# Performance work log

Measured on AMD Instinct MI355X. Metric: run time of the kernel, lower is better.

Reference implementation:

```python
import jax, jax.numpy as jnp
import numpy as np

N, M, H, DIN, DOUT = 65536, 512, 1024, 512, 512
EPS = 1e-8


def setup_inputs() -> dict:
    key = jax.random.key(0)
    ks = jax.random.split(key, 24)
    s = 0.02  # weight init scale
    f32 = jnp.float32
    inp = {
        "x": jax.random.normal(ks[0], (DIN,), f32),
        "h0": jax.random.normal(ks[1], (H,), f32),
        "c0": jax.random.normal(ks[2], (H,), f32),
        "memory": jax.random.normal(ks[3], (N, M), f32),
        "read_vec": jax.random.normal(ks[4], (M,), f32),
        # LSTMCell params (torch layout: gates ordered i, f, g, o)
        "W_ih": jax.random.normal(ks[5], (4 * H, DIN + M), f32) * s,
        "b_ih": jax.random.normal(ks[6], (4 * H,), f32) * s,
        "W_hh": jax.random.normal(ks[7], (4 * H, H), f32) * s,
        "b_hh": jax.random.normal(ks[8], (4 * H,), f32) * s,
        # output head
        "W_fc": jax.random.normal(ks[9], (DOUT, H), f32) * s,
        "b_fc": jax.random.normal(ks[10], (DOUT,), f32) * s,
        # addressing / write heads
        "W_key": jax.random.normal(ks[11], (M, H), f32) * s,
        "b_key": jax.random.normal(ks[12], (M,), f32) * s,
        "W_beta": jax.random.normal(ks[13], (1, H), f32) * s,
        "b_beta": jax.random.normal(ks[14], (1,), f32) * s,
        "W_erase": jax.random.normal(ks[15], (M, H), f32) * s,
        "b_erase": jax.random.normal(ks[16], (M,), f32) * s,
        "W_add": jax.random.normal(ks[17], (M, H), f32) * s,
        "b_add": jax.random.normal(ks[18], (M,), f32) * s,
    }
    return inp


def reference(x, h0, c0, memory, read_vec,
              W_ih, b_ih, W_hh, b_hh, W_fc, b_fc,
              W_key, b_key, W_beta, b_beta,
              W_erase, b_erase, W_add, b_add):
    # controller input: cat([x, prev read vector])  -> [DIN + M]
    xi = jnp.concatenate([x, read_vec])
    # LSTMCell (torch gate order i, f, g, o)
    gates = W_ih @ xi + b_ih + W_hh @ h0 + b_hh  # [4H]
    i, f, g, o = jnp.split(gates, 4)
    i = jax.nn.sigmoid(i)
    f = jax.nn.sigmoid(f)
    g = jnp.tanh(g)
    o = jax.nn.sigmoid(o)
    c = f * c0 + i * g
    h = o * jnp.tanh(c)
    out = jax.nn.sigmoid(W_fc @ h + b_fc)  # sigmoid(controller_out)

    # content addressing on the PRE-write memory
    kvec = jnp.tanh(W_key @ h + b_key)                       # [M]
    beta = jax.nn.softplus(W_beta @ h + b_beta) + EPS        # [1]
    kn = kvec / (jnp.linalg.norm(kvec) + EPS)                # global-norm key (as in source)
    mem_norm = memory / (jnp.linalg.norm(memory, axis=1, keepdims=True) + EPS)  # [N,M]
    sim = mem_norm @ kn                                       # [N]
    w = jax.nn.softmax(beta * sim)                            # [N]

    # write (erase then add), then read from the UPDATED memory
    erase = jax.nn.sigmoid(W_erase @ h + b_erase)             # [M]
    add = jnp.tanh(W_add @ h + b_add)                         # [M]
    mem_new = memory * (1.0 - w[:, None] * erase[None, :]) + w[:, None] * add[None, :]
    read_new = w @ mem_new                                    # [M]
    return (out, h, c, mem_new, read_new)
```

## Files before the change

kernel.cpp:

```cpp
#include <hip/hip_runtime.h>
#include <math.h>

#define N_ROWS 65536
#define M_DIM  512
#define H_DIM  1024
#define EPS    1e-8f
#define NBLK_U 2048
#define NBLK_S 2048

typedef float f32x4 __attribute__((ext_vector_type(4)));

__device__ __forceinline__ float sigmoidf_(float v) { return 1.f / (1.f + expf(-v)); }

#define WS_KVEC  0
#define WS_ERASE 512
#define WS_ADD   1024
#define WS_SCAL  1536
#define WS_P     2048
#define WS_PSUM  67584
#define WS_PART  69632
#define WS_OUT1  1118208

__global__ void __launch_bounds__(256) k_gatecell(
        const float* __restrict__ x, const float* __restrict__ rv,
        const float* __restrict__ h0, const float* __restrict__ c0,
        const float* __restrict__ W_ih, const float* __restrict__ b_ih,
        const float* __restrict__ W_hh, const float* __restrict__ b_hh,
        float* __restrict__ h_out, float* __restrict__ c_out) {
    __shared__ float gval[4];
    int j = blockIdx.x;
    int wid = threadIdx.x >> 6;
    int lane = threadIdx.x & 63;
    int r = wid * H_DIM + j;
    const float4* Wi = (const float4*)(W_ih + (size_t)r * 1024);
    const float4* Wh = (const float4*)(W_hh + (size_t)r * 1024);
    const float4* xv = (const float4*)x;
    const float4* rvv = (const float4*)rv;
    const float4* hv = (const float4*)h0;
    float s = 0.f;
#pragma unroll
    for (int k = 0; k < 4; ++k) {
        int idx = k * 64 + lane;
        float4 wiv = Wi[idx];
        float4 in4 = (k < 2) ? xv[idx] : rvv[idx - 128];
        s += wiv.x * in4.x + wiv.y * in4.y + wiv.z * in4.z + wiv.w * in4.w;
        float4 whv = Wh[idx];
        float4 h4 = hv[idx];
        s += whv.x * h4.x + whv.y * h4.y + whv.z * h4.z + whv.w * h4.w;
    }
#pragma unroll
    for (int o = 32; o > 0; o >>= 1) s += __shfl_xor(s, o);
    if (lane == 0) gval[wid] = s + b_ih[r] + b_hh[r];
    __syncthreads();
    if (threadIdx.x == 0) {
        float ig = sigmoidf_(gval[0]);
        float fg = sigmoidf_(gval[1]);
        float gg = tanhf(gval[2]);
        float og = sigmoidf_(gval[3]);
        float c = fg * c0[j] + ig * gg;
        float h = og * tanhf(c);
        c_out[j] = c;
        h_out[j] = h;
    }
}

__global__ void __launch_bounds__(256) k_heads(
        const float* __restrict__ h,
        const float* __restrict__ W_fc, const float* __restrict__ b_fc,
        const float* __restrict__ W_key, const float* __restrict__ b_key,
        const float* __restrict__ W_beta, const float* __restrict__ b_beta,
        const float* __restrict__ W_erase, const float* __restrict__ b_erase,
        const float* __restrict__ W_add, const float* __restrict__ b_add,
        float* __restrict__ out, float* __restrict__ kvec,
        float* __restrict__ scal, float* __restrict__ erase,
        float* __restrict__ addv) {
    int wave = (blockIdx.x * blockDim.x + threadIdx.x) >> 6;
    int lane = threadIdx.x & 63;
    if (wave >= 2049) return;
    const float* Wrow;
    float bias;
    int kind, r;
    if (wave < 512)        { kind = 0; r = wave;        Wrow = W_fc    + (size_t)r * 1024; bias = b_fc[r]; }
    else if (wave < 1024)  { kind = 1; r = wave - 512;  Wrow = W_key   + (size_t)r * 1024; bias = b_key[r]; }
    else if (wave == 1024) { kind = 2; r = 0;           Wrow = W_beta;                     bias = b_beta[0]; }
    else if (wave < 1537)  { kind = 3; r = wave - 1025; Wrow = W_erase + (size_t)r * 1024; bias = b_erase[r]; }
    else                   { kind = 4; r = wave - 1537; Wrow = W_add   + (size_t)r * 1024; bias = b_add[r]; }
    const float4* Wv = (const float4*)Wrow;
    const float4* hv = (const float4*)h;
    float s = 0.f;
#pragma unroll
    for (int k = 0; k < 4; ++k) {
        int idx = k * 64 + lane;
        float4 w4 = Wv[idx];
        float4 h4 = hv[idx];
        s += w4.x * h4.x + w4.y * h4.y + w4.z * h4.z + w4.w * h4.w;
    }
#pragma unroll
    for (int o = 32; o > 0; o >>= 1) s += __shfl_xor(s, o);
    if (lane == 0) {
        float v = s + bias;
        if (kind == 0)      out[r]   = sigmoidf_(v);
        else if (kind == 1) kvec[r]  = tanhf(v);
        else if (kind == 2) scal[0]  = v;
        else if (kind == 3) erase[r] = sigmoidf_(v);
        else                addv[r]  = tanhf(v);
    }
}

__global__ void __launch_bounds__(256) k_simexp(
        const float* __restrict__ mem, const float* __restrict__ kvec,
        const float* __restrict__ scal,
        float* __restrict__ p, float* __restrict__ psum) {
    __shared__ float red[256];
    __shared__ float skn[512];
    __shared__ float wsum[4];
    int t = threadIdx.x;
    float v0 = kvec[t];
    float v1 = kvec[t + 256];
    red[t] = v0 * v0 + v1 * v1;
    __syncthreads();
#pragma unroll
    for (int s2 = 128; s2 > 0; s2 >>= 1) {
        if (t < s2) red[t] += red[t + s2];
        __syncthreads();
    }
    float invn = 1.f / (sqrtf(red[0]) + EPS);
    float braw = scal[0];
    float beta = ((braw > 20.f) ? braw : log1pf(expf(braw))) + EPS;
    skn[t] = v0 * invn;
    skn[t + 256] = v1 * invn;
    __syncthreads();
    int wid = t >> 6, lane = t & 63;
    float4 k0 = ((const float4*)skn)[lane];
    float4 k1 = ((const float4*)skn)[64 + lane];
    int gw = blockIdx.x * 4 + wid;
    size_t base = (size_t)gw * 8;
    float lsum = 0.f;
#pragma unroll 2
    for (int i = 0; i < 8; ++i) {
        size_t row = base + i;
        const float4* mv = (const float4*)(mem + row * M_DIM);
        float4 m0 = mv[lane];
        float4 m1 = mv[64 + lane];
        float dot = m0.x * k0.x + m0.y * k0.y + m0.z * k0.z + m0.w * k0.w
                  + m1.x * k1.x + m1.y * k1.y + m1.z * k1.z + m1.w * k1.w;
        float ss  = m0.x * m0.x + m0.y * m0.y + m0.z * m0.z + m0.w * m0.w
                  + m1.x * m1.x + m1.y * m1.y + m1.z * m1.z + m1.w * m1.w;
#pragma unroll
        for (int o = 32; o > 0; o >>= 1) {
            dot += __shfl_xor(dot, o);
            ss  += __shfl_xor(ss, o);
        }
        float pe = expf(beta * (dot / (sqrtf(ss) + EPS)));
        if (lane == 0) {
            p[row] = pe;
            lsum += pe;
        }
    }
    if (lane == 0) wsum[wid] = lsum;
    __syncthreads();
    if (t == 0) psum[blockIdx.x] = (wsum[0] + wsum[1]) + (wsum[2] + wsum[3]);
}

__global__ void __launch_bounds__(256) k_update(
        const float* __restrict__ mem, const float* __restrict__ p,
        const float* __restrict__ psum,
        const float* __restrict__ erase, const float* __restrict__ addv,
        float* __restrict__ mem_out, float* __restrict__ partial) {
    __shared__ float red[256];
    __shared__ float4 s_e[128];
    __shared__ float4 s_a[128];
    __shared__ float  s_w[32];
    __shared__ float4 s_red[128];
    int t = threadIdx.x;
    float s = 0.f;
#pragma unroll
    for (int i = 0; i < 8; ++i) s += psum[t + i * 256];
    red[t] = s;
    __syncthreads();
#pragma unroll
    for (int s2 = 128; s2 > 0; s2 >>= 1) {
        if (t < s2) red[t] += red[t + s2];
        __syncthreads();
    }
    float winv = 1.f / red[0];
    if (t < 128) {
        s_e[t] = ((const float4*)erase)[t];
        s_a[t] = ((const float4*)addv)[t];
    }
    int rowBase = blockIdx.x * 32;
    if (t < 32) s_w[t] = p[rowBase + t] * winv;
    __syncthreads();
    int sub = t >> 7;
    int c4  = t & 127;
    float4 e4 = s_e[c4];
    float4 a4 = s_a[c4];
    float4 acc = make_float4(0.f, 0.f, 0.f, 0.f);
#pragma unroll 4
    for (int it = 0; it < 16; ++it) {
        int row = rowBase + it * 2 + sub;
        float wr = s_w[it * 2 + sub];
        float4 m4 = ((const float4*)(mem + (size_t)row * M_DIM))[c4];
        f32x4 n4;
        n4.x = m4.x * (1.f - wr * e4.x) + wr * a4.x;
        n4.y = m4.y * (1.f - wr * e4.y) + wr * a4.y;
        n4.z = m4.z * (1.f - wr * e4.z) + wr * a4.z;
        n4.w = m4.w * (1.f - wr * e4.w) + wr * a4.w;
        __builtin_nontemporal_store(n4, (f32x4*)(mem_out + (size_t)row * M_DIM) + c4);
        acc.x += wr * n4.x;
        acc.y += wr * n4.y;
        acc.z += wr * n4.z;
        acc.w += wr * n4.w;
    }
    if (sub) s_red[c4] = acc;
    __syncthreads();
    if (!sub) {
        float4 o = s_red[c4];
        acc.x += o.x; acc.y += o.y; acc.z += o.z; acc.w += o.w;
        ((float4*)(partial + (size_t)blockIdx.x * M_DIM))[c4] = acc;
    }
}

__global__ void __launch_bounds__(256) k_red1(const float* __restrict__ partial,
                                              float* __restrict__ out1) {
    int g = blockIdx.x, t = threadIdx.x;
    float s0 = 0.f, s1 = 0.f;
    int b0 = g * 32;
#pragma unroll 4
    for (int b = b0; b < b0 + 32; ++b) {
        s0 += partial[(size_t)b * M_DIM + t];
        s1 += partial[(size_t)b * M_DIM + 256 + t];
    }
    out1[(size_t)g * M_DIM + t] = s0;
    out1[(size_t)g * M_DIM + 256 + t] = s1;
}

__global__ void __launch_bounds__(512) k_red2(const float* __restrict__ out1,
                                              float* __restrict__ read_new) {
    int t = threadIdx.x;
    float s = 0.f;
#pragma unroll 4
    for (int g = 0; g < 64; ++g) s += out1[(size_t)g * M_DIM + t];
    read_new[t] = s;
}

extern "C" void kernel_launch(void* const* d_in, const int* in_sizes, int n_in,
                              void* d_out, int out_size, void* d_ws, size_t ws_size,
                              hipStream_t stream) {
    const float* x        = (const float*)d_in[0];
    const float* h0       = (const float*)d_in[1];
    const float* c0       = (const float*)d_in[2];
    const float* memory   = (const float*)d_in[3];
    const float* read_vec = (const float*)d_in[4];
    const float* W_ih     = (const float*)d_in[5];
    const float* b_ih     = (const float*)d_in[6];
    const float* W_hh     = (const float*)d_in[7];
    const float* b_hh     = (const float*)d_in[8];
    const float* W_fc     = (const float*)d_in[9];
    const float* b_fc     = (const float*)d_in[10];
    const float* W_key    = (const float*)d_in[11];
    const float* b_key    = (const float*)d_in[12];
    const float* W_beta   = (const float*)d_in[13];
    const float* b_beta   = (const float*)d_in[14];
    const float* W_erase  = (const float*)d_in[15];
    const float* b_erase  = (const float*)d_in[16];
    const float* W_add    = (const float*)d_in[17];
    const float* b_add    = (const float*)d_in[18];

    float* out      = (float*)d_out;
    float* h_out    = out + 512;
    float* c_out    = h_out + 1024;
    float* mem_out  = c_out + 1024;
    float* read_out = mem_out + (size_t)N_ROWS * M_DIM;

    float* ws     = (float*)d_ws;
    float* kvec   = ws + WS_KVEC;
    float* erase  = ws + WS_ERASE;
    float* addv   = ws + WS_ADD;
    float* scal   = ws + WS_SCAL;
    float* p      = ws + WS_P;
    float* psum   = ws + WS_PSUM;
    float* part   = ws + WS_PART;
    float* out1   = ws + WS_OUT1;

    k_gatecell<<<1024, 256, 0, stream>>>(x, read_vec, h0, c0, W_ih, b_ih, W_hh, b_hh,
                                         h_out, c_out);
    k_heads<<<513, 256, 0, stream>>>(h_out, W_fc, b_fc, W_key, b_key, W_beta, b_beta,
                                     W_erase, b_erase, W_add, b_add,
                                     out, kvec, scal, erase, addv);
    k_simexp<<<NBLK_S, 256, 0, stream>>>(memory, kvec, scal, p, psum);
    k_update<<<NBLK_U, 256, 0, stream>>>(memory, p, psum, erase, addv, mem_out, part);
    k_red1<<<64, 256, 0, stream>>>(part, out1);
    k_red2<<<1, 512, 0, stream>>>(out1, read_out);
}
```

Measured before the change: 91.17 us.

## Compute read vector algebraically from pre-write memory during similarity pass

Expands read_new = w·mem_new into sum(p·m)/S - erase·sum(p²·m)/S² + add·sum(p²)/S², accumulating the two weighted row sums while memory is already loaded for the similarity pass. The update kernel becomes a pure streaming write with no reduction, and the final merge applies the normalisation. Similarity blocks now handle 16 rows each with more registers and shared memory, and rounding differs from the direct formula.

```diff
diff --git a/kernel.cpp b/kernel.cpp
--- a/kernel.cpp
+++ b/kernel.cpp
@@ -5,8 +5,8 @@
 #define M_DIM  512
 #define H_DIM  1024
 #define EPS    1e-8f
+#define NBLK_S 1024
 #define NBLK_U 2048
-#define NBLK_S 2048
 
 typedef float f32x4 __attribute__((ext_vector_type(4)));
 
@@ -18,8 +18,11 @@
 #define WS_SCAL  1536
 #define WS_P     2048
 #define WS_PSUM  67584
-#define WS_PART  69632
-#define WS_OUT1  1118208
+#define WS_P2SUM 68608
+#define WS_PART1 69632
+#define WS_PART2 593920
+#define WS_O1A   1118208
+#define WS_O1B   1150976
 
 __global__ void __launch_bounds__(256) k_gatecell(
         const float* __restrict__ x, const float* __restrict__ rv,
@@ -110,18 +113,22 @@
 __global__ void __launch_bounds__(256) k_simexp(
         const float* __restrict__ mem, const float* __restrict__ kvec,
         const float* __restrict__ scal,
-        float* __restrict__ p, float* __restrict__ psum) {
+        float* __restrict__ p, float* __restrict__ psum, float* __restrict__ p2sum,
+        float* __restrict__ part1, float* __restrict__ part2) {
     __shared__ float red[256];
     __shared__ float skn[512];
     __shared__ float wsum[4];
+    __shared__ float w2sum[4];
+    __shared__ float4 s1[4][128];
+    __shared__ float4 s2[4][128];
     int t = threadIdx.x;
     float v0 = kvec[t];
     float v1 = kvec[t + 256];
     red[t] = v0 * v0 + v1 * v1;
     __syncthreads();
 #pragma unroll
-    for (int s2 = 128; s2 > 0; s2 >>= 1) {
-        if (t < s2) red[t] += red[t + s2];
+    for (int s2_ = 128; s2_ > 0; s2_ >>= 1) {
+        if (t < s2_) red[t] += red[t + s2_];
         __syncthreads();
     }
     float invn = 1.f / (sqrtf(red[0]) + EPS);
@@ -133,11 +140,12 @@
     int wid = t >> 6, lane = t & 63;
     float4 k0 = ((const float4*)skn)[lane];
     float4 k1 = ((const float4*)skn)[64 + lane];
-    int gw = blockIdx.x * 4 + wid;
-    size_t base = (size_t)gw * 8;
-    float lsum = 0.f;
+    size_t base = ((size_t)blockIdx.x * 4 + wid) * 16;
+    float lsum = 0.f, l2sum = 0.f;
+    float4 a1lo = make_float4(0.f,0.f,0.f,0.f), a1hi = make_float4(0.f,0.f,0.f,0.f);
+    float4 a2lo = make_float4(0.f,0.f,0.f,0.f), a2hi = make_float4(0.f,0.f,0.f,0.f);
 #pragma unroll 2
-    for (int i = 0; i < 8; ++i) {
+    for (int i = 0; i < 16; ++i) {
         size_t row = base + i;
         const float4* mv = (const float4*)(mem + row * M_DIM);
         float4 m0 = mv[lane];
@@ -152,35 +160,61 @@
             ss  += __shfl_xor(ss, o);
         }
         float pe = expf(beta * (dot / (sqrtf(ss) + EPS)));
-        if (lane == 0) {
-            p[row] = pe;
-            lsum += pe;
-        }
-    }
-    if (lane == 0) wsum[wid] = lsum;
-    __syncthreads();
-    if (t == 0) psum[blockIdx.x] = (wsum[0] + wsum[1]) + (wsum[2] + wsum[3]);
+        if (lane == 0) p[row] = pe;
+        float pe2 = pe * pe;
+        lsum += pe;
+        l2sum += pe2;
+        a1lo.x += pe * m0.x;  a1lo.y += pe * m0.y;  a1lo.z += pe * m0.z;  a1lo.w += pe * m0.w;
+        a1hi.x += pe * m1.x;  a1hi.y += pe * m1.y;  a1hi.z += pe * m1.z;  a1hi.w += pe * m1.w;
+        a2lo.x += pe2 * m0.x; a2lo.y += pe2 * m0.y; a2lo.z += pe2 * m0.z; a2lo.w += pe2 * m0.w;
+        a2hi.x += pe2 * m1.x; a2hi.y += pe2 * m1.y; a2hi.z += pe2 * m1.z; a2hi.w += pe2 * m1.w;
+    }
+    s1[wid][lane] = a1lo;  s1[wid][64 + lane] = a1hi;
+    s2[wid][lane] = a2lo;  s2[wid][64 + lane] = a2hi;
+    if (lane == 0) { wsum[wid] = lsum; w2sum[wid] = l2sum; }
+    __syncthreads();
+    if (t < 128) {
+        float4 A = s1[0][t], B = s1[1][t], C = s1[2][t], D = s1[3][t];
+        float4 r4;
+        r4.x = (A.x + B.x) + (C.x + D.x);
+        r4.y = (A.y + B.y) + (C.y + D.y);
+        r4.z = (A.z + B.z) + (C.z + D.z);
+        r4.w = (A.w + B.w) + (C.w + D.w);
+        ((float4*)(part1 + (size_t)blockIdx.x * M_DIM))[t] = r4;
+    } else {
+        int u = t - 128;
+        float4 A = s2[0][u], B = s2[1][u], C = s2[2][u], D = s2[3][u];
+        float4 r4;
+        r4.x = (A.x + B.x) + (C.x + D.x);
+        r4.y = (A.y + B.y) + (C.y + D.y);
+        r4.z = (A.z + B.z) + (C.z + D.z);
+        r4.w = (A.w + B.w) + (C.w + D.w);
+        ((float4*)(part2 + (size_t)blockIdx.x * M_DIM))[u] = r4;
+    }
+    if (t == 0) {
+        psum[blockIdx.x]  = (wsum[0] + wsum[1]) + (wsum[2] + wsum[3]);
+        p2sum[blockIdx.x] = (w2sum[0] + w2sum[1]) + (w2sum[2] + w2sum[3]);
+    }
 }
 
 __global__ void __launch_bounds__(256) k_update(
         const float* __restrict__ mem, const float* __restrict__ p,
         const float* __restrict__ psum,
         const float* __restrict__ erase, const float* __restrict__ addv,
-        float* __restrict__ mem_out, float* __restrict__ partial) {
+        float* __restrict__ mem_out) {
     __shared__ float red[256];
     __shared__ float4 s_e[128];
     __shared__ float4 s_a[128];
     __shared__ float  s_w[32];
-    __shared__ float4 s_red[128];
     int t = threadIdx.x;
     float s = 0.f;
 #pragma unroll
-    for (int i = 0; i < 8; ++i) s += psum[t + i * 256];
+    for (int i = 0; i < 4; ++i) s += psum[t + i * 256];
     red[t] = s;
     __syncthreads();
 #pragma unroll
-    for (int s2 = 128; s2 > 0; s2 >>= 1) {
-        if (t < s2) red[t] += red[t + s2];
+    for (int s2_ = 128; s2_ > 0; s2_ >>= 1) {
+        if (t < s2_) red[t] += red[t + s2_];
         __syncthreads();
     }
     float winv = 1.f / red[0];
@@ -195,7 +229,6 @@
     int c4  = t & 127;
     float4 e4 = s_e[c4];
     float4 a4 = s_a[c4];
-    float4 acc = make_float4(0.f, 0.f, 0.f, 0.f);
 #pragma unroll 4
     for (int it = 0; it < 16; ++it) {
         int row = rowBase + it * 2 + sub;
@@ -207,41 +240,61 @@
         n4.z = m4.z * (1.f - wr * e4.z) + wr * a4.z;
         n4.w = m4.w * (1.f - wr * e4.w) + wr * a4.w;
         __builtin_nontemporal_store(n4, (f32x4*)(mem_out + (size_t)row * M_DIM) + c4);
-        acc.x += wr * n4.x;
-        acc.y += wr * n4.y;
-        acc.z += wr * n4.z;
-        acc.w += wr * n4.w;
-    }
-    if (sub) s_red[c4] = acc;
-    __syncthreads();
-    if (!sub) {
-        float4 o = s_red[c4];
-        acc.x += o.x; acc.y += o.y; acc.z += o.z; acc.w += o.w;
-        ((float4*)(partial + (size_t)blockIdx.x * M_DIM))[c4] = acc;
-    }
-}
-
-__global__ void __launch_bounds__(256) k_red1(const float* __restrict__ partial,
-                                              float* __restrict__ out1) {
+    }
+}
+
+__global__ void __launch_bounds__(256) k_merge1(
+        const float* __restrict__ part1, const float* __restrict__ part2,
+        float* __restrict__ o1a, float* __restrict__ o1b) {
     int g = blockIdx.x, t = threadIdx.x;
-    float s0 = 0.f, s1 = 0.f;
-    int b0 = g * 32;
+    float s0 = 0.f, s1 = 0.f, s2 = 0.f, s3 = 0.f;
+    int b0 = g * 16;
 #pragma unroll 4
-    for (int b = b0; b < b0 + 32; ++b) {
-        s0 += partial[(size_t)b * M_DIM + t];
-        s1 += partial[(size_t)b * M_DIM + 256 + t];
-    }
-    out1[(size_t)g * M_DIM + t] = s0;
-    out1[(size_t)g * M_DIM + 256 + t] = s1;
-}
-
-__global__ void __launch_bounds__(512) k_red2(const float* __restrict__ out1,
-                                              float* __restrict__ read_new) {
+    for (int b = b0; b < b0 + 16; ++b) {
+        s0 += part1[(size_t)b * M_DIM + t];
+        s1 += part1[(size_t)b * M_DIM + 256 + t];
+        s2 += part2[(size_t)b * M_DIM + t];
+        s3 += part2[(size_t)b * M_DIM + 256 + t];
+    }
+    o1a[(size_t)g * M_DIM + t] = s0;
+    o1a[(size_t)g * M_DIM + 256 + t] = s1;
+    o1b[(size_t)g * M_DIM + t] = s2;
+    o1b[(size_t)g * M_DIM + 256 + t] = s3;
+}
+
+__global__ void __launch_bounds__(512) k_merge2(
+        const float* __restrict__ o1a, const float* __restrict__ o1b,
+        const float* __restrict__ psum, const float* __restrict__ p2sum,
+        const float* __restrict__ erase, const float* __restrict__ addv,
+        float* __restrict__ read_new) {
+    __shared__ float red[512];
     int t = threadIdx.x;
-    float s = 0.f;
+    red[t] = psum[t] + psum[t + 512];
+    __syncthreads();
+#pragma unroll
+    for (int s2_ = 256; s2_ > 0; s2_ >>= 1) {
+        if (t < s2_) red[t] += red[t + s2_];
+        __syncthreads();
+    }
+    float sumP = red[0];
+    __syncthreads();
+    red[t] = p2sum[t] + p2sum[t + 512];
+    __syncthreads();
+#pragma unroll
+    for (int s2_ = 256; s2_ > 0; s2_ >>= 1) {
+        if (t < s2_) red[t] += red[t + s2_];
+        __syncthreads();
+    }
+    float sumP2 = red[0];
+    float invS  = 1.f / sumP;
+    float invSS = invS * invS;
+    float r1 = 0.f, r2 = 0.f;
 #pragma unroll 4
-    for (int g = 0; g < 64; ++g) s += out1[(size_t)g * M_DIM + t];
-    read_new[t] = s;
+    for (int g = 0; g < 64; ++g) {
+        r1 += o1a[(size_t)g * M_DIM + t];
+        r2 += o1b[(size_t)g * M_DIM + t];
+    }
+    read_new[t] = r1 * invS - erase[t] * r2 * invSS + addv[t] * sumP2 * invSS;
 }
 
 extern "C" void kernel_launch(void* const* d_in, const int* in_sizes, int n_in,
@@ -280,16 +333,19 @@
     float* scal   = ws + WS_SCAL;
     float* p      = ws + WS_P;
     float* psum   = ws + WS_PSUM;
-    float* part   = ws + WS_PART;
-    float* out1   = ws + WS_OUT1;
+    float* p2sum  = ws + WS_P2SUM;
+    float* part1  = ws + WS_PART1;
+    float* part2  = ws + WS_PART2;
+    float* o1a    = ws + WS_O1A;
+    float* o1b    = ws + WS_O1B;
 
     k_gatecell<<<1024, 256, 0, stream>>>(x, read_vec, h0, c0, W_ih, b_ih, W_hh, b_hh,
                                          h_out, c_out);
     k_heads<<<513, 256, 0, stream>>>(h_out, W_fc, b_fc, W_key, b_key, W_beta, b_beta,
                                      W_erase, b_erase, W_add, b_add,
                                      out, kvec, scal, erase, addv);
-    k_simexp<<<NBLK_S, 256, 0, stream>>>(memory, kvec, scal, p, psum);
-    k_update<<<NBLK_U, 256, 0, stream>>>(memory, p, psum, erase, addv, mem_out, part);
-    k_red1<<<64, 256, 0, stream>>>(part, out1);
-    k_red2<<<1, 512, 0, stream>>>(out1, read_out);
-}
+    k_simexp<<<NBLK_S, 256, 0, stream>>>(memory, kvec, scal, p, psum, p2sum, part1, part2);
+    k_update<<<NBLK_U, 256, 0, stream>>>(memory, p, psum, erase, addv, mem_out);
+    k_merge1<<<64, 256, 0, stream>>>(part1, part2, o1a, o1b);
+    k_merge2<<<1, 512, 0, stream>>>(o1a, o1b, psum, p2sum, erase, addv, read_out);
+}
```

New measurement: 91.91 us. Within noise of the previous version (+0.8%).

## Compute read vector algebraically in similarity pass with fixed-point atomics

Applied to the files above, without the earlier changes.

Expands read_new = w @ mem_new algebraically into sums of p*mem, p^2*mem, sum p and sum p^2, all accumulated in the similarity kernel while memory rows are already in registers. The partials go into 64-bit fixed-point atomics, which keeps the result deterministic, and the accumulator is zeroed by spare waves in the heads kernel. This removes the read accumulation from the update kernel and drops the two reduction kernels, cutting launches and partial traffic. The costs are extra FMAs and block-level atomics in k_simexp, and fixed-point quantization (scale 2^26) could lose precision or overflow for large exponent values.

```diff
diff --git a/kernel.cpp b/kernel.cpp
--- a/kernel.cpp
+++ b/kernel.cpp
@@ -5,21 +5,25 @@
 #define M_DIM  512
 #define H_DIM  1024
 #define EPS    1e-8f
+#define NBLK_S 1024
 #define NBLK_U 2048
-#define NBLK_S 2048
 
 typedef float f32x4 __attribute__((ext_vector_type(4)));
+typedef unsigned long long u64;
+
+#define FX_SCALE 67108864.0f
+#define FX_INV   (1.0 / 67108864.0)
 
 __device__ __forceinline__ float sigmoidf_(float v) { return 1.f / (1.f + expf(-v)); }
+__device__ __forceinline__ u64 fx_(float v) { return (u64)(long long)llrintf(v * FX_SCALE); }
+__device__ __forceinline__ float unfx_(u64 v) { return (float)((double)(long long)v * FX_INV); }
 
 #define WS_KVEC  0
 #define WS_ERASE 512
 #define WS_ADD   1024
 #define WS_SCAL  1536
 #define WS_P     2048
-#define WS_PSUM  67584
-#define WS_PART  69632
-#define WS_OUT1  1118208
+#define WS_ACC   67584
 
 __global__ void __launch_bounds__(256) k_gatecell(
         const float* __restrict__ x, const float* __restrict__ rv,
@@ -73,10 +77,14 @@
         const float* __restrict__ W_add, const float* __restrict__ b_add,
         float* __restrict__ out, float* __restrict__ kvec,
         float* __restrict__ scal, float* __restrict__ erase,
-        float* __restrict__ addv) {
+        float* __restrict__ addv, u64* __restrict__ acc) {
     int wave = (blockIdx.x * blockDim.x + threadIdx.x) >> 6;
     int lane = threadIdx.x & 63;
-    if (wave >= 2049) return;
+    if (wave >= 2049) {
+        int z = threadIdx.x - 64;
+        for (int i = z; i < 1026; i += 192) acc[i] = 0ULL;
+        return;
+    }
     const float* Wrow;
     float bias;
     int kind, r;
@@ -110,18 +118,21 @@
 __global__ void __launch_bounds__(256) k_simexp(
         const float* __restrict__ mem, const float* __restrict__ kvec,
         const float* __restrict__ scal,
-        float* __restrict__ p, float* __restrict__ psum) {
+        float* __restrict__ p, u64* __restrict__ acc) {
     __shared__ float red[256];
     __shared__ float skn[512];
     __shared__ float wsum[4];
+    __shared__ float w2sum[4];
+    __shared__ float4 s1[4][128];
+    __shared__ float4 s2[4][128];
     int t = threadIdx.x;
     float v0 = kvec[t];
     float v1 = kvec[t + 256];
     red[t] = v0 * v0 + v1 * v1;
     __syncthreads();
 #pragma unroll
-    for (int s2 = 128; s2 > 0; s2 >>= 1) {
-        if (t < s2) red[t] += red[t + s2];
+    for (int s2_ = 128; s2_ > 0; s2_ >>= 1) {
+        if (t < s2_) red[t] += red[t + s2_];
         __syncthreads();
     }
     float invn = 1.f / (sqrtf(red[0]) + EPS);
@@ -133,11 +144,12 @@
     int wid = t >> 6, lane = t & 63;
     float4 k0 = ((const float4*)skn)[lane];
     float4 k1 = ((const float4*)skn)[64 + lane];
-    int gw = blockIdx.x * 4 + wid;
-    size_t base = (size_t)gw * 8;
-    float lsum = 0.f;
+    size_t base = ((size_t)blockIdx.x * 4 + wid) * 16;
+    float lsum = 0.f, l2sum = 0.f;
+    float4 a1lo = make_float4(0.f,0.f,0.f,0.f), a1hi = make_float4(0.f,0.f,0.f,0.f);
+    float4 a2lo = make_float4(0.f,0.f,0.f,0.f), a2hi = make_float4(0.f,0.f,0.f,0.f);
 #pragma unroll 2
-    for (int i = 0; i < 8; ++i) {
+    for (int i = 0; i < 16; ++i) {
         size_t row = base + i;
         const float4* mv = (const float4*)(mem + row * M_DIM);
         float4 m0 = mv[lane];
@@ -152,38 +164,52 @@
             ss  += __shfl_xor(ss, o);
         }
         float pe = expf(beta * (dot / (sqrtf(ss) + EPS)));
-        if (lane == 0) {
-            p[row] = pe;
-            lsum += pe;
-        }
-    }
-    if (lane == 0) wsum[wid] = lsum;
-    __syncthreads();
-    if (t == 0) psum[blockIdx.x] = (wsum[0] + wsum[1]) + (wsum[2] + wsum[3]);
+        if (lane == 0) p[row] = pe;
+        float pe2 = pe * pe;
+        lsum += pe;
+        l2sum += pe2;
+        a1lo.x += pe * m0.x;  a1lo.y += pe * m0.y;  a1lo.z += pe * m0.z;  a1lo.w += pe * m0.w;
+        a1hi.x += pe * m1.x;  a1hi.y += pe * m1.y;  a1hi.z += pe * m1.z;  a1hi.w += pe * m1.w;
+        a2lo.x += pe2 * m0.x; a2lo.y += pe2 * m0.y; a2lo.z += pe2 * m0.z; a2lo.w += pe2 * m0.w;
+        a2hi.x += pe2 * m1.x; a2hi.y += pe2 * m1.y; a2hi.z += pe2 * m1.z; a2hi.w += pe2 * m1.w;
+    }
+    s1[wid][lane] = a1lo;  s1[wid][64 + lane] = a1hi;
+    s2[wid][lane] = a2lo;  s2[wid][64 + lane] = a2hi;
+    if (lane == 0) { wsum[wid] = lsum; w2sum[wid] = l2sum; }
+    __syncthreads();
+    if (t < 128) {
+        float4 A = s1[0][t], B = s1[1][t], C = s1[2][t], D = s1[3][t];
+        u64* R1 = acc + 2;
+        atomicAdd(&R1[4*t + 0], fx_((A.x + B.x) + (C.x + D.x)));
+        atomicAdd(&R1[4*t + 1], fx_((A.y + B.y) + (C.y + D.y)));
+        atomicAdd(&R1[4*t + 2], fx_((A.z + B.z) + (C.z + D.z)));
+        atomicAdd(&R1[4*t + 3], fx_((A.w + B.w) + (C.w + D.w)));
+    } else {
+        int u = t - 128;
+        float4 A = s2[0][u], B = s2[1][u], C = s2[2][u], D = s2[3][u];
+        u64* R2 = acc + 514;
+        atomicAdd(&R2[4*u + 0], fx_((A.x + B.x) + (C.x + D.x)));
+        atomicAdd(&R2[4*u + 1], fx_((A.y + B.y) + (C.y + D.y)));
+        atomicAdd(&R2[4*u + 2], fx_((A.z + B.z) + (C.z + D.z)));
+        atomicAdd(&R2[4*u + 3], fx_((A.w + B.w) + (C.w + D.w)));
+    }
+    if (t == 0) {
+        atomicAdd(&acc[0], fx_((wsum[0] + wsum[1]) + (wsum[2] + wsum[3])));
+        atomicAdd(&acc[1], fx_((w2sum[0] + w2sum[1]) + (w2sum[2] + w2sum[3])));
+    }
 }
 
 __global__ void __launch_bounds__(256) k_update(
         const float* __restrict__ mem, const float* __restrict__ p,
-        const float* __restrict__ psum,
+        const u64* __restrict__ acc,
         const float* __restrict__ erase, const float* __restrict__ addv,
-        float* __restrict__ mem_out, float* __restrict__ partial) {
-    __shared__ float red[256];
+        float* __restrict__ mem_out, float* __restrict__ read_out) {
     __shared__ float4 s_e[128];
     __shared__ float4 s_a[128];
     __shared__ float  s_w[32];
-    __shared__ float4 s_red[128];
     int t = threadIdx.x;
-    float s = 0.f;
-#pragma unroll
-    for (int i = 0; i < 8; ++i) s += psum[t + i * 256];
-    red[t] = s;
-    __syncthreads();
-#pragma unroll
-    for (int s2 = 128; s2 > 0; s2 >>= 1) {
-        if (t < s2) red[t] += red[t + s2];
-        __syncthreads();
-    }
-    float winv = 1.f / red[0];
+    float S = unfx_(acc[0]);
+    float winv = 1.f / S;
     if (t < 128) {
         s_e[t] = ((const float4*)erase)[t];
         s_a[t] = ((const float4*)addv)[t];
@@ -195,7 +221,6 @@
     int c4  = t & 127;
     float4 e4 = s_e[c4];
     float4 a4 = s_a[c4];
-    float4 acc = make_float4(0.f, 0.f, 0.f, 0.f);
 #pragma unroll 4
     for (int it = 0; it < 16; ++it) {
         int row = rowBase + it * 2 + sub;
@@ -207,41 +232,17 @@
         n4.z = m4.z * (1.f - wr * e4.z) + wr * a4.z;
         n4.w = m4.w * (1.f - wr * e4.w) + wr * a4.w;
         __builtin_nontemporal_store(n4, (f32x4*)(mem_out + (size_t)row * M_DIM) + c4);
-        acc.x += wr * n4.x;
-        acc.y += wr * n4.y;
-        acc.z += wr * n4.z;
-        acc.w += wr * n4.w;
-    }
-    if (sub) s_red[c4] = acc;
-    __syncthreads();
-    if (!sub) {
-        float4 o = s_red[c4];
-        acc.x += o.x; acc.y += o.y; acc.z += o.z; acc.w += o.w;
-        ((float4*)(partial + (size_t)blockIdx.x * M_DIM))[c4] = acc;
-    }
-}
-
-__global__ void __launch_bounds__(256) k_red1(const float* __restrict__ partial,
-                                              float* __restrict__ out1) {
-    int g = blockIdx.x, t = threadIdx.x;
-    float s0 = 0.f, s1 = 0.f;
-    int b0 = g * 32;
-#pragma unroll 4
-    for (int b = b0; b < b0 + 32; ++b) {
-        s0 += partial[(size_t)b * M_DIM + t];
-        s1 += partial[(size_t)b * M_DIM + 256 + t];
-    }
-    out1[(size_t)g * M_DIM + t] = s0;
-    out1[(size_t)g * M_DIM + 256 + t] = s1;
-}
-
-__global__ void __launch_bounds__(512) k_red2(const float* __restrict__ out1,
-                                              float* __restrict__ read_new) {
-    int t = threadIdx.x;
-    float s = 0.f;
-#pragma unroll 4
-    for (int g = 0; g < 64; ++g) s += out1[(size_t)g * M_DIM + t];
-    read_new[t] = s;
+    }
+    if (blockIdx.x == 0) {
+        float sumP2 = unfx_(acc[1]);
+        float invSS = winv * winv;
+#pragma unroll
+        for (int m = t; m < 512; m += 256) {
+            float r1 = unfx_(acc[2 + m]);
+            float r2 = unfx_(acc[514 + m]);
+            read_out[m] = r1 * winv - erase[m] * r2 * invSS + addv[m] * sumP2 * invSS;
+        }
+    }
 }
 
 extern "C" void kernel_launch(void* const* d_in, const int* in_sizes, int n_in,
@@ -279,17 +280,13 @@
     float* addv   = ws + WS_ADD;
     float* scal   = ws + WS_SCAL;
     float* p      = ws + WS_P;
-    float* psum   = ws + WS_PSUM;
-    float* part   = ws + WS_PART;
-    float* out1   = ws + WS_OUT1;
+    u64*   acc    = (u64*)(ws + WS_ACC);
 
     k_gatecell<<<1024, 256, 0, stream>>>(x, read_vec, h0, c0, W_ih, b_ih, W_hh, b_hh,
                                          h_out, c_out);
     k_heads<<<513, 256, 0, stream>>>(h_out, W_fc, b_fc, W_key, b_key, W_beta, b_beta,
                                      W_erase, b_erase, W_add, b_add,
-                                     out, kvec, scal, erase, addv);
-    k_simexp<<<NBLK_S, 256, 0, stream>>>(memory, kvec, scal, p, psum);
-    k_update<<<NBLK_U, 256, 0, stream>>>(memory, p, psum, erase, addv, mem_out, part);
-    k_red1<<<64, 256, 0, stream>>>(part, out1);
-    k_red2<<<1, 512, 0, stream>>>(out1, read_out);
-}
+                                     out, kvec, scal, erase, addv, acc);
+    k_simexp<<<NBLK_S, 256, 0, stream>>>(memory, kvec, scal, p, acc);
+    k_update<<<NBLK_U, 256, 0, stream>>>(memory, p, acc, erase, addv, mem_out, read_out);
+}
```

Result: slower. 175.0 us (+91.9%).
